# Optimization experiments

Hardware: AMD Instinct MI355X
Metric: run time of the kernel (lower is better)

The kernel has to match this reference:

```python
import jax, jax.numpy as jnp
import numpy as np

N_NODES = 50000
N_EDGES = 800000
WIDTH = 128
N_EDGE_FEATS = 2


def setup_inputs() -> dict:
    key = jax.random.key(0)
    k = jax.random.split(key, 6)
    x_p = jax.random.normal(k[0], (N_NODES, WIDTH), dtype=jnp.float32)
    edge_indices = jax.random.randint(k[1], (2, N_EDGES), 0, N_NODES, dtype=jnp.int64 if jax.config.jax_enable_x64 else jnp.int32)
    edge_feats = jax.random.normal(k[2], (N_EDGES, N_EDGE_FEATS), dtype=jnp.float32)
    # LinearBlock params: Linear + ReLU (batch_norm=False, dropout=0)
    W_edge = jax.random.normal(k[3], (WIDTH + N_EDGE_FEATS, WIDTH), dtype=jnp.float32) * (1.0 / np.sqrt(WIDTH + N_EDGE_FEATS))
    b_edge = jnp.zeros((WIDTH,), dtype=jnp.float32)
    W_mlp = jax.random.normal(k[4], (2 * WIDTH, WIDTH), dtype=jnp.float32) * (1.0 / np.sqrt(2 * WIDTH))
    b_mlp = jnp.zeros((WIDTH,), dtype=jnp.float32)
    return {"x_p": x_p, "edge_indices": edge_indices, "edge_feats": edge_feats,
            "W_edge": W_edge, "b_edge": b_edge, "W_mlp": W_mlp, "b_mlp": b_mlp}


def reference(x_p, edge_indices, edge_feats, W_edge, b_edge, W_mlp, b_mlp):
    n = x_p.shape[0]
    # Symmetrize edges: cat([e, flip(e, dims=0)], dim=1) -> [2, 2E]
    e_src = jnp.concatenate([edge_indices[0], edge_indices[1]], axis=0)
    e_dst = jnp.concatenate([edge_indices[1], edge_indices[0]], axis=0)
    ef = jnp.concatenate([edge_feats, edge_feats], axis=0)          # [2E, F]
    # gather -> diff
    diffs = x_p[e_dst] - x_p[e_src]                                  # [2E, W]
    # edge MLP with residual: e_feat = diffs + relu(cat([diffs, ef]) @ W + b)
    h = jax.nn.relu(jnp.concatenate([diffs, ef], axis=1) @ W_edge + b_edge)
    e_val = diffs + h                                                # [2E, W]
    # scatter_max back to nodes; empty segments -> 0 (torch_scatter convention)
    maxes = jax.ops.segment_max(e_val, e_dst, num_segments=n)        # [N, W]
    maxes = jnp.where(jnp.isfinite(maxes), maxes, jnp.zeros_like(maxes))
    # node MLP with residual
    out = x_p + jax.nn.relu(jnp.concatenate([x_p, maxes], axis=1) @ W_mlp + b_mlp)
    return out
```

## Files before the change

kernel.cpp:

```cpp
#include <hip/hip_runtime.h>
#include <math.h>

#define WD 128
#define BSH 3
#define BN 8
#define CAP 384

typedef short bf16x8 __attribute__((ext_vector_type(8)));
typedef float f32x4 __attribute__((ext_vector_type(4)));

__device__ __forceinline__ unsigned bf16_rne(float f) {
    unsigned u = __float_as_uint(f);
    return (u + 0x7FFFu + ((u >> 16) & 1u)) >> 16;
}
__device__ __forceinline__ float bf16_lo(unsigned p) {
    return __uint_as_float(p << 16);
}
__device__ __forceinline__ float bf16_hi(unsigned p) {
    return __uint_as_float(p & 0xFFFF0000u);
}
__device__ __forceinline__ float bf16_us(unsigned short s) {
    return __uint_as_float(((unsigned)s) << 16);
}

__global__ __launch_bounds__(512) void k_prep(const float* __restrict__ We,
                                              unsigned short* __restrict__ wsT) {
    int t = blockIdx.x * 512 + threadIdx.x;
    if (t < WD * WD) {
        int k = t >> 7, c = t & 127;
        wsT[c * WD + k] = (unsigned short)bf16_rne(We[t]);
    }
}

__global__ __launch_bounds__(512) void k_fused(const float* __restrict__ x,
                                               const unsigned short* __restrict__ wsT,
                                               unsigned* __restrict__ xy,
                                               const int* __restrict__ ei,
                                               const float* __restrict__ ef,
                                               int* __restrict__ bcur,
                                               int2* __restrict__ adj2,
                                               int n, int E, int gb) {
    __shared__ unsigned short xs_bf[32][136];
    if ((int)blockIdx.x < gb) {
        int row0 = (int)blockIdx.x * 32;
        for (int t = threadIdx.x; t < 32 * WD; t += 512) {
            int r = t >> 7, c = t & 127;
            int gr = row0 + r;
            xs_bf[r][c] = (gr < n) ? (unsigned short)bf16_rne(x[(size_t)gr * WD + c]) : 0;
        }
        __syncthreads();
        int l = threadIdx.x & 63;
        int w = threadIdx.x >> 6;
        int cl = l & 15;
        int kg = l >> 4;
        int c0 = w * 16;
        f32x4 acc0 = {0.f, 0.f, 0.f, 0.f};
        f32x4 acc1 = {0.f, 0.f, 0.f, 0.f};
        const unsigned short* wcol = wsT + (size_t)(c0 + cl) * WD;
        #pragma unroll
        for (int ks = 0; ks < 4; ++ks) {
            int k0 = ks * 32 + kg * 8;
            bf16x8 a0 = *(const bf16x8*)&xs_bf[cl][k0];
            bf16x8 a1 = *(const bf16x8*)&xs_bf[16 + cl][k0];
            bf16x8 b  = *(const bf16x8*)&wcol[k0];
            acc0 = __builtin_amdgcn_mfma_f32_16x16x32_bf16(a0, b, acc0, 0, 0, 0);
            acc1 = __builtin_amdgcn_mfma_f32_16x16x32_bf16(a1, b, acc1, 0, 0, 0);
        }
        #pragma unroll
        for (int r = 0; r < 4; ++r) {
            int row = kg * 4 + r;
            int gr = row0 + row;
            if (gr < n)
                xy[(size_t)gr * WD + c0 + cl] =
                    (unsigned)xs_bf[row][c0 + cl] | (bf16_rne(acc0[r]) << 16);
            int row2 = row + 16;
            int gr2 = row0 + row2;
            if (gr2 < n)
                xy[(size_t)gr2 * WD + c0 + cl] =
                    (unsigned)xs_bf[row2][c0 + cl] | (bf16_rne(acc1[r]) << 16);
        }
    } else {
        int base = (((int)blockIdx.x - gb) * 512 + (int)threadIdx.x) * 2;
        if (base + 2 <= E) {
            int2 a = *(const int2*)(ei + base);
            int2 b = *(const int2*)(ei + E + base);
            float4 f = *(const float4*)(ef + 2 * base);
            int ep0 = (int)(bf16_rne(f.x) | (bf16_rne(f.y) << 16));
            int ep1 = (int)(bf16_rne(f.z) | (bf16_rne(f.w) << 16));
            int p0 = atomicAdd(&bcur[b.x >> BSH], 1);
            int p1 = atomicAdd(&bcur[a.x >> BSH], 1);
            int p2 = atomicAdd(&bcur[b.y >> BSH], 1);
            int p3 = atomicAdd(&bcur[a.y >> BSH], 1);
            int2 v;
            if (p0 < CAP) { v.x = a.x | ((b.x & 7) << 20); v.y = ep0;
                            adj2[(size_t)(b.x >> BSH) * CAP + p0] = v; }
            if (p1 < CAP) { v.x = b.x | ((a.x & 7) << 20); v.y = ep0;
                            adj2[(size_t)(a.x >> BSH) * CAP + p1] = v; }
            if (p2 < CAP) { v.x = a.y | ((b.y & 7) << 20); v.y = ep1;
                            adj2[(size_t)(b.y >> BSH) * CAP + p2] = v; }
            if (p3 < CAP) { v.x = b.y | ((a.y & 7) << 20); v.y = ep1;
                            adj2[(size_t)(a.y >> BSH) * CAP + p3] = v; }
        } else {
            for (int e = base; e < E; ++e) {
                int aa = ei[e];
                int bb = ei[E + e];
                float2 ff = ((const float2*)ef)[e];
                int efp = (int)(bf16_rne(ff.x) | (bf16_rne(ff.y) << 16));
                int q1 = atomicAdd(&bcur[bb >> BSH], 1);
                if (q1 < CAP) { int2 v; v.x = aa | ((bb & 7) << 20); v.y = efp;
                                adj2[(size_t)(bb >> BSH) * CAP + q1] = v; }
                int q2 = atomicAdd(&bcur[aa >> BSH], 1);
                if (q2 < CAP) { int2 v; v.x = bb | ((aa & 7) << 20); v.y = efp;
                                adj2[(size_t)(aa >> BSH) * CAP + q2] = v; }
            }
        }
    }
}

__global__ __launch_bounds__(128) void k_nodemax_out(const int* __restrict__ bcnt,
                                                     const int2* __restrict__ adj2,
                                                     const unsigned* __restrict__ xy,
                                                     const float* __restrict__ We,
                                                     const float* __restrict__ be,
                                                     const float* __restrict__ Wm,
                                                     const float* __restrict__ bm,
                                                     float* __restrict__ out, int n) {
    __shared__ int2 sh[CAP];
    __shared__ unsigned xyd[BN][WD];
    __shared__ unsigned short mxs[BN][WD];
    __shared__ int hist[BN];
    int bkt = blockIdx.x;
    int j = threadIdx.x;
    int node0 = bkt * BN;
    int cnt = bcnt[bkt];
    cnt = min(cnt, CAP);
    if (j < BN) hist[j] = 0;
    #pragma unroll
    for (int dl = 0; dl < BN; ++dl) {
        int nd = node0 + dl;
        xyd[dl][j] = (nd < n) ? xy[(size_t)nd * WD + j] : 0u;
    }
    size_t base = (size_t)bkt * CAP;
    __syncthreads();
    int2 e0, e1, e2;
    int d0 = -1, d1 = -1, d2 = -1;
    if (j < cnt)       { e0 = adj2[base + j];       d0 = e0.x >> 20; atomicAdd(&hist[d0], 1); }
    if (j + 128 < cnt) { e1 = adj2[base + j + 128]; d1 = e1.x >> 20; atomicAdd(&hist[d1], 1); }
    if (j + 256 < cnt) { e2 = adj2[base + j + 256]; d2 = e2.x >> 20; atomicAdd(&hist[d2], 1); }
    __syncthreads();
    if (j == 0) {
        int s = 0;
        #pragma unroll
        for (int d = 0; d < BN; ++d) { int t = hist[d]; hist[d] = s; s += t; }
    }
    __syncthreads();
    if (d0 >= 0) { int p = atomicAdd(&hist[d0], 1); sh[p] = e0; }
    if (d1 >= 0) { int p = atomicAdd(&hist[d1], 1); sh[p] = e1; }
    if (d2 >= 0) { int p = atomicAdd(&hist[d2], 1); sh[p] = e2; }
    __syncthreads();
    float w0 = We[128 * WD + j];
    float w1 = We[129 * WD + j];
    float bj = be[j];
    int sbeg = 0;
    #pragma unroll
    for (int dl = 0; dl < BN; ++dl) {
        int send = hist[dl];
        unsigned q = xyd[dl][j];
        float xdl = bf16_lo(q), ydl = bf16_hi(q);
        float m = -INFINITY;
        int i = sbeg;
        for (; i + 4 <= send; i += 4) {
            int2 v0 = sh[i], v1 = sh[i + 1], v2 = sh[i + 2], v3 = sh[i + 3];
            unsigned p0 = xy[(size_t)(v0.x & 0xFFFFF) * WD + j];
            unsigned p1 = xy[(size_t)(v1.x & 0xFFFFF) * WD + j];
            unsigned p2 = xy[(size_t)(v2.x & 0xFFFFF) * WD + j];
            unsigned p3 = xy[(size_t)(v3.x & 0xFFFFF) * WD + j];
            unsigned ee0 = (unsigned)v0.y, ee1 = (unsigned)v1.y;
            unsigned ee2 = (unsigned)v2.y, ee3 = (unsigned)v3.y;
            float c0 = fmaf(bf16_lo(ee0), w0, fmaf(bf16_hi(ee0), w1, bj));
            float c1 = fmaf(bf16_lo(ee1), w0, fmaf(bf16_hi(ee1), w1, bj));
            float c2 = fmaf(bf16_lo(ee2), w0, fmaf(bf16_hi(ee2), w1, bj));
            float c3 = fmaf(bf16_lo(ee3), w0, fmaf(bf16_hi(ee3), w1, bj));
            float u0 = (xdl - bf16_lo(p0)) + fmaxf((ydl - bf16_hi(p0)) + c0, 0.f);
            float u1 = (xdl - bf16_lo(p1)) + fmaxf((ydl - bf16_hi(p1)) + c1, 0.f);
            float u2 = (xdl - bf16_lo(p2)) + fmaxf((ydl - bf16_hi(p2)) + c2, 0.f);
            float u3 = (xdl - bf16_lo(p3)) + fmaxf((ydl - bf16_hi(p3)) + c3, 0.f);
            m = fmaxf(m, fmaxf(fmaxf(u0, u1), fmaxf(u2, u3)));
        }
        for (; i < send; ++i) {
            int2 v0 = sh[i];
            unsigned p0 = xy[(size_t)(v0.x & 0xFFFFF) * WD + j];
            unsigned ee0 = (unsigned)v0.y;
            float c0 = fmaf(bf16_lo(ee0), w0, fmaf(bf16_hi(ee0), w1, bj));
            m = fmaxf(m, (xdl - bf16_lo(p0)) + fmaxf((ydl - bf16_hi(p0)) + c0, 0.f));
        }
        mxs[dl][j] = (unsigned short)bf16_rne((send > sbeg) ? m : 0.f);
        sbeg = send;
    }
    __syncthreads();
    float acc[BN] = {0.f, 0.f, 0.f, 0.f, 0.f, 0.f, 0.f, 0.f};
    #pragma unroll 2
    for (int k4 = 0; k4 < 32; ++k4) {
        float wa = Wm[(4 * k4 + 0) * WD + j];
        float wb = Wm[(4 * k4 + 1) * WD + j];
        float wc = Wm[(4 * k4 + 2) * WD + j];
        float wd = Wm[(4 * k4 + 3) * WD + j];
        #pragma unroll
        for (int dl = 0; dl < BN; ++dl) {
            uint4 xq = ((const uint4*)xyd[dl])[k4];
            acc[dl] = fmaf(bf16_lo(xq.x), wa, fmaf(bf16_lo(xq.y), wb,
                      fmaf(bf16_lo(xq.z), wc, fmaf(bf16_lo(xq.w), wd, acc[dl]))));
        }
    }
    #pragma unroll 2
    for (int k4 = 0; k4 < 32; ++k4) {
        float wa = Wm[(128 + 4 * k4 + 0) * WD + j];
        float wb = Wm[(128 + 4 * k4 + 1) * WD + j];
        float wc = Wm[(128 + 4 * k4 + 2) * WD + j];
        float wd = Wm[(128 + 4 * k4 + 3) * WD + j];
        #pragma unroll
        for (int dl = 0; dl < BN; ++dl) {
            ushort4 mq = ((const ushort4*)mxs[dl])[k4];
            acc[dl] = fmaf(bf16_us(mq.x), wa, fmaf(bf16_us(mq.y), wb,
                      fmaf(bf16_us(mq.z), wc, fmaf(bf16_us(mq.w), wd, acc[dl]))));
        }
    }
    float bmj = bm[j];
    #pragma unroll
    for (int dl = 0; dl < BN; ++dl) {
        int nd = node0 + dl;
        if (nd < n) {
            float xv = bf16_lo(xyd[dl][j]);
            out[(size_t)nd * WD + j] = xv + fmaxf(acc[dl] + bmj, 0.f);
        }
    }
}

extern "C" void kernel_launch(void* const* d_in, const int* in_sizes, int n_in,
                              void* d_out, int out_size, void* d_ws, size_t ws_size,
                              hipStream_t stream) {
    const float* x_p = (const float*)d_in[0];
    const int*   ei  = (const int*)d_in[1];
    const float* ef  = (const float*)d_in[2];
    const float* We  = (const float*)d_in[3];
    const float* be  = (const float*)d_in[4];
    const float* Wm  = (const float*)d_in[5];
    const float* bm  = (const float*)d_in[6];

    int n = in_sizes[0] / WD;
    int E = in_sizes[1] / 2;
    int nb = (n + BN - 1) / BN;

    char* p = (char*)d_ws;
    unsigned* xy = (unsigned*)p;          p += (size_t)n * WD * sizeof(unsigned);
    int* bcur = (int*)p;                  p += ((size_t)nb * 4 + 15) & ~15ull;
    int2* adj2 = (int2*)p;                p += (size_t)nb * CAP * 8;
    unsigned short* wsT = (unsigned short*)p; p += (size_t)WD * WD * 2;

    int gb = (n + 31) / 32;
    int sb = (E + 1023) / 1024;

    hipMemsetAsync(bcur, 0, (size_t)nb * sizeof(int), stream);
    k_prep<<<32, 512, 0, stream>>>(We, wsT);
    k_fused<<<gb + sb, 512, 0, stream>>>(x_p, wsT, xy, ei, ef, bcur, adj2, n, E, gb);
    k_nodemax_out<<<nb, 128, 0, stream>>>(bcur, adj2, xy, We, be, Wm, bm,
                                          (float*)d_out, n);
}
```

Before: 283.6 us.

## Split node MLP into separate bf16 MFMA GEMM kernel

The node-output MLP moves out of the scatter-max kernel, which used scalar FMAs with fp32 weights read per thread, into a new kernel that computes it with bf16 MFMA 16x16x32 on 32-row tiles. The per-node maxima are written as bf16 into the first slots of each bucket's adjacency buffer, overwriting data the bucket has already consumed, and the new kernel reads them back. Wm is transposed and converted to bf16 in the prep kernel. This adds a kernel launch and a global round-trip for the maxima, in exchange for removing the register- and FMA-heavy tail from the gather kernel.

```diff
diff --git a/kernel.cpp b/kernel.cpp
--- a/kernel.cpp
+++ b/kernel.cpp
@@ -24,11 +24,18 @@
 }
 
 __global__ __launch_bounds__(512) void k_prep(const float* __restrict__ We,
-                                              unsigned short* __restrict__ wsT) {
+                                              const float* __restrict__ Wm,
+                                              unsigned short* __restrict__ wsT,
+                                              unsigned short* __restrict__ wmT) {
     int t = blockIdx.x * 512 + threadIdx.x;
     if (t < WD * WD) {
         int k = t >> 7, c = t & 127;
         wsT[c * WD + k] = (unsigned short)bf16_rne(We[t]);
+    }
+    int t2 = t - WD * WD;
+    if (t2 >= 0 && t2 < 2 * WD * WD) {
+        int k = t2 >> 7, c = t2 & 127;
+        wmT[c * 2 * WD + k] = (unsigned short)bf16_rne(Wm[t2]);
     }
 }
 
@@ -117,17 +124,14 @@
     }
 }
 
-__global__ __launch_bounds__(128) void k_nodemax_out(const int* __restrict__ bcnt,
-                                                     const int2* __restrict__ adj2,
-                                                     const unsigned* __restrict__ xy,
-                                                     const float* __restrict__ We,
-                                                     const float* __restrict__ be,
-                                                     const float* __restrict__ Wm,
-                                                     const float* __restrict__ bm,
-                                                     float* __restrict__ out, int n) {
+__global__ __launch_bounds__(128) void k_nodemax(const int* __restrict__ bcnt,
+                                                 int2* __restrict__ adj2,
+                                                 const unsigned* __restrict__ xy,
+                                                 const float* __restrict__ We,
+                                                 const float* __restrict__ be,
+                                                 int n) {
     __shared__ int2 sh[CAP];
     __shared__ unsigned xyd[BN][WD];
-    __shared__ unsigned short mxs[BN][WD];
     __shared__ int hist[BN];
     int bkt = blockIdx.x;
     int j = threadIdx.x;
@@ -161,6 +165,7 @@
     float w0 = We[128 * WD + j];
     float w1 = We[129 * WD + j];
     float bj = be[j];
+    unsigned short* mrow = (unsigned short*)(adj2 + base);
     int sbeg = 0;
     #pragma unroll
     for (int dl = 0; dl < BN; ++dl) {
@@ -194,45 +199,65 @@
             float c0 = fmaf(bf16_lo(ee0), w0, fmaf(bf16_hi(ee0), w1, bj));
             m = fmaxf(m, (xdl - bf16_lo(p0)) + fmaxf((ydl - bf16_hi(p0)) + c0, 0.f));
         }
-        mxs[dl][j] = (unsigned short)bf16_rne((send > sbeg) ? m : 0.f);
+        mrow[dl * WD + j] = (unsigned short)bf16_rne((send > sbeg) ? m : 0.f);
         sbeg = send;
     }
-    __syncthreads();
-    float acc[BN] = {0.f, 0.f, 0.f, 0.f, 0.f, 0.f, 0.f, 0.f};
-    #pragma unroll 2
-    for (int k4 = 0; k4 < 32; ++k4) {
-        float wa = Wm[(4 * k4 + 0) * WD + j];
-        float wb = Wm[(4 * k4 + 1) * WD + j];
-        float wc = Wm[(4 * k4 + 2) * WD + j];
-        float wd = Wm[(4 * k4 + 3) * WD + j];
-        #pragma unroll
-        for (int dl = 0; dl < BN; ++dl) {
-            uint4 xq = ((const uint4*)xyd[dl])[k4];
-            acc[dl] = fmaf(bf16_lo(xq.x), wa, fmaf(bf16_lo(xq.y), wb,
-                      fmaf(bf16_lo(xq.z), wc, fmaf(bf16_lo(xq.w), wd, acc[dl]))));
-        }
-    }
-    #pragma unroll 2
-    for (int k4 = 0; k4 < 32; ++k4) {
-        float wa = Wm[(128 + 4 * k4 + 0) * WD + j];
-        float wb = Wm[(128 + 4 * k4 + 1) * WD + j];
-        float wc = Wm[(128 + 4 * k4 + 2) * WD + j];
-        float wd = Wm[(128 + 4 * k4 + 3) * WD + j];
-        #pragma unroll
-        for (int dl = 0; dl < BN; ++dl) {
-            ushort4 mq = ((const ushort4*)mxs[dl])[k4];
-            acc[dl] = fmaf(bf16_us(mq.x), wa, fmaf(bf16_us(mq.y), wb,
-                      fmaf(bf16_us(mq.z), wc, fmaf(bf16_us(mq.w), wd, acc[dl]))));
-        }
-    }
-    float bmj = bm[j];
-    #pragma unroll
-    for (int dl = 0; dl < BN; ++dl) {
-        int nd = node0 + dl;
-        if (nd < n) {
-            float xv = bf16_lo(xyd[dl][j]);
-            out[(size_t)nd * WD + j] = xv + fmaxf(acc[dl] + bmj, 0.f);
-        }
+}
+
+__global__ __launch_bounds__(512) void k_gemm_out(const unsigned* __restrict__ xy,
+                                                  const int2* __restrict__ adj2,
+                                                  const unsigned short* __restrict__ wmT,
+                                                  const float* __restrict__ bm,
+                                                  float* __restrict__ out, int n) {
+    __shared__ unsigned short As[32][264];
+    int row0 = (int)blockIdx.x * 32;
+    for (int t = threadIdx.x; t < 32 * WD; t += 512) {
+        int r = t >> 7, c = t & 127;
+        int gr = row0 + r;
+        As[r][c] = (gr < n) ? (unsigned short)(xy[(size_t)gr * WD + c] & 0xFFFFu) : 0;
+    }
+    for (int t = threadIdx.x; t < 32 * WD; t += 512) {
+        int r = t >> 7, c = t & 127;
+        int gr = row0 + r;
+        unsigned short v = 0;
+        if (gr < n) {
+            const unsigned short* mrow =
+                (const unsigned short*)(adj2 + (size_t)(gr >> 3) * CAP) + (gr & 7) * WD;
+            v = mrow[c];
+        }
+        As[r][WD + c] = v;
+    }
+    __syncthreads();
+    int l = threadIdx.x & 63;
+    int w = threadIdx.x >> 6;
+    int cl = l & 15;
+    int kg = l >> 4;
+    int c0 = w * 16;
+    f32x4 acc0 = {0.f, 0.f, 0.f, 0.f};
+    f32x4 acc1 = {0.f, 0.f, 0.f, 0.f};
+    const unsigned short* wcol = wmT + (size_t)(c0 + cl) * 256;
+    #pragma unroll
+    for (int ks = 0; ks < 8; ++ks) {
+        int k0 = ks * 32 + kg * 8;
+        bf16x8 a0 = *(const bf16x8*)&As[cl][k0];
+        bf16x8 a1 = *(const bf16x8*)&As[16 + cl][k0];
+        bf16x8 b  = *(const bf16x8*)&wcol[k0];
+        acc0 = __builtin_amdgcn_mfma_f32_16x16x32_bf16(a0, b, acc0, 0, 0, 0);
+        acc1 = __builtin_amdgcn_mfma_f32_16x16x32_bf16(a1, b, acc1, 0, 0, 0);
+    }
+    float bmv = bm[c0 + cl];
+    #pragma unroll
+    for (int r = 0; r < 4; ++r) {
+        int row = kg * 4 + r;
+        int gr = row0 + row;
+        if (gr < n)
+            out[(size_t)gr * WD + c0 + cl] =
+                bf16_us(As[row][c0 + cl]) + fmaxf(acc0[r] + bmv, 0.f);
+        int row2 = row + 16;
+        int gr2 = row0 + row2;
+        if (gr2 < n)
+            out[(size_t)gr2 * WD + c0 + cl] =
+                bf16_us(As[row2][c0 + cl]) + fmaxf(acc1[r] + bmv, 0.f);
     }
 }
 
@@ -256,13 +281,14 @@
     int* bcur = (int*)p;                  p += ((size_t)nb * 4 + 15) & ~15ull;
     int2* adj2 = (int2*)p;                p += (size_t)nb * CAP * 8;
     unsigned short* wsT = (unsigned short*)p; p += (size_t)WD * WD * 2;
+    unsigned short* wmT = (unsigned short*)p; p += (size_t)WD * 2 * WD * 2;
 
     int gb = (n + 31) / 32;
     int sb = (E + 1023) / 1024;
 
     hipMemsetAsync(bcur, 0, (size_t)nb * sizeof(int), stream);
-    k_prep<<<32, 512, 0, stream>>>(We, wsT);
+    k_prep<<<96, 512, 0, stream>>>(We, Wm, wsT, wmT);
     k_fused<<<gb + sb, 512, 0, stream>>>(x_p, wsT, xy, ei, ef, bcur, adj2, n, E, gb);
-    k_nodemax_out<<<nb, 128, 0, stream>>>(bcur, adj2, xy, We, be, Wm, bm,
-                                          (float*)d_out, n);
-}
+    k_nodemax<<<nb, 128, 0, stream>>>(bcur, adj2, xy, We, be, n);
+    k_gemm_out<<<gb, 512, 0, stream>>>(xy, adj2, wmT, bm, (float*)d_out, n);
+}
```

After: 244.8 us. 1.16x faster.
